# Performance work log

Measured on AMD Instinct MI355X. Metric: run time of the kernel, lower is better.

## Reference

```python
import jax, jax.numpy as jnp
import numpy as np

N, B, T, S, E, R = 4, 8, 512, 512, 1024, 1024


def setup_inputs() -> dict:
    key = jax.random.key(0)
    k1, k2, k3, k4, k5 = jax.random.split(key, 5)
    return {
        "query": jax.random.normal(k1, (1, B, T, E), dtype=jnp.float32),
        "key_value_states": jax.random.normal(k2, (N, B, S, R), dtype=jnp.float32),
        "attention_mask": jax.random.normal(k3, (1, B, T, S), dtype=jnp.float32),
        "Wk": jax.random.normal(k4, (E, R), dtype=jnp.float32) * (1.0 / np.sqrt(R)),
        "bk": jax.random.normal(k5, (E,), dtype=jnp.float32) * 0.01,
    }


def reference(query, key_value_states, attention_mask, Wk, bk):
    # k_proj: [N,B,S,R] @ [R,E] + bias -> [N,B,S,E]
    key = jnp.einsum("nbsr,er->nbse", key_value_states, Wk) + bk
    # QK^T (no scaling), query broadcast over N: [N,B,T,S]
    scores = jnp.einsum("bte,nbse->nbts", query[0], key)
    scores = scores + attention_mask  # mask broadcast over N
    attn = jax.nn.softmax(scores, axis=-1)
    # weights @ raw key_value_states (NOT projected key): [N,B,T,R]
    out = jnp.einsum("nbts,nbsr->nbtr", attn, key_value_states)
    return out
```

## Files before the change

### kernel.cpp

```cpp
#include <hip/hip_runtime.h>

typedef unsigned short u16;
typedef unsigned int u32;
typedef unsigned long long u64;

typedef __bf16 bfrag __attribute__((ext_vector_type(8)));
typedef float f32x4 __attribute__((ext_vector_type(4)));

typedef __attribute__((address_space(1))) char* gas1_p;
typedef __attribute__((address_space(3))) char* las3_p;

#define DI __device__ __forceinline__

DI u16 f2bf(float f) {
  u32 u = __float_as_uint(f);
  u += 0x7FFFu + ((u >> 16) & 1u);
  return (u16)(u >> 16);
}
DI float bf2f(u16 h) { return __uint_as_float(((u32)h) << 16); }

DI void gload16(const void* g, void* l) {
  __builtin_amdgcn_global_load_lds((gas1_p)(u64)g, (las3_p)(u32)(u64)l, 16, 0, 0);
}

__global__ __launch_bounds__(256) void k_split4(const float4* __restrict__ in,
                                                uint2* __restrict__ hi,
                                                uint2* __restrict__ lo) {
  int i = blockIdx.x * 256 + threadIdx.x;
  float4 v = in[i];
  u16 h0 = f2bf(v.x), h1 = f2bf(v.y), h2 = f2bf(v.z), h3 = f2bf(v.w);
  u16 l0 = f2bf(v.x - bf2f(h0)), l1 = f2bf(v.y - bf2f(h1));
  u16 l2 = f2bf(v.z - bf2f(h2)), l3 = f2bf(v.w - bf2f(h3));
  hi[i] = make_uint2((u32)h0 | ((u32)h1 << 16), (u32)h2 | ((u32)h3 << 16));
  lo[i] = make_uint2((u32)l0 | ((u32)l1 << 16), (u32)l2 | ((u32)l3 << 16));
}

template <int WH, int WTH, int WTL>
__global__ __launch_bounds__(256) void k_trsplit64(const float* __restrict__ in,
                                                   u16* __restrict__ hi, u16* __restrict__ lo,
                                                   u16* __restrict__ thi, u16* __restrict__ tlo,
                                                   int rows, int cols) {
  __shared__ float tile[64][65];
  const u64 zoff = (u64)blockIdx.z * (u64)rows * (u64)cols;
  const int r0 = threadIdx.x >> 4;
  const int c4 = (threadIdx.x & 15) << 2;
  const float* src = in + zoff + (u64)(blockIdx.y * 64 + r0) * cols + blockIdx.x * 64 + c4;
#pragma unroll
  for (int p = 0; p < 4; ++p) {
    float4 v = *reinterpret_cast<const float4*>(src + (u64)(p * 16) * cols);
    tile[r0 + p * 16][c4 + 0] = v.x;
    tile[r0 + p * 16][c4 + 1] = v.y;
    tile[r0 + p * 16][c4 + 2] = v.z;
    tile[r0 + p * 16][c4 + 3] = v.w;
  }
  __syncthreads();
  if constexpr (WH) {
    const int rr = threadIdx.x >> 3;
    const int cc = (threadIdx.x & 7) << 3;
#pragma unroll
    for (int p = 0; p < 2; ++p) {
      const int r = rr + p * 32;
      u32 h[4], l[4];
#pragma unroll
      for (int j = 0; j < 4; ++j) {
        float a = tile[r][cc + 2 * j], b = tile[r][cc + 2 * j + 1];
        u16 ha = f2bf(a), hb = f2bf(b);
        h[j] = (u32)ha | ((u32)hb << 16);
        l[j] = (u32)f2bf(a - bf2f(ha)) | ((u32)f2bf(b - bf2f(hb)) << 16);
      }
      const u64 o = zoff + (u64)(blockIdx.y * 64 + r) * cols + blockIdx.x * 64 + cc;
      *reinterpret_cast<uint4*>(hi + o) = make_uint4(h[0], h[1], h[2], h[3]);
      *reinterpret_cast<uint4*>(lo + o) = make_uint4(l[0], l[1], l[2], l[3]);
    }
  }
  if constexpr (WTH) {
#pragma unroll
    for (int p = 0; p < 2; ++p) {
      const int id = threadIdx.x + p * 256;
      const int col = id >> 3;
      const int s8 = (id & 7) << 3;
      u32 h[4], l[4];
#pragma unroll
      for (int j = 0; j < 4; ++j) {
        float a = tile[s8 + 2 * j][col], b = tile[s8 + 2 * j + 1][col];
        u16 ha = f2bf(a), hb = f2bf(b);
        h[j] = (u32)ha | ((u32)hb << 16);
        if constexpr (WTL)
          l[j] = (u32)f2bf(a - bf2f(ha)) | ((u32)f2bf(b - bf2f(hb)) << 16);
      }
      const u64 o = zoff + (u64)(blockIdx.x * 64 + col) * rows + blockIdx.y * 64 + s8;
      *reinterpret_cast<uint4*>(thi + o) = make_uint4(h[0], h[1], h[2], h[3]);
      if constexpr (WTL)
        *reinterpret_cast<uint4*>(tlo + o) = make_uint4(l[0], l[1], l[2], l[3]);
    }
  }
}

template <int X3, int SPLITOUT, int ADDMASK, int XT, int YT>
__global__ __launch_bounds__(256, 2) void k_gemm_bt(
    const u16* __restrict__ Ah, const u16* __restrict__ Al,
    const u16* __restrict__ Bh, const u16* __restrict__ Bl,
    float* __restrict__ Cf, u16* __restrict__ Chi, u16* __restrict__ Clo,
    const float* __restrict__ Mask,
    int K, int N, u64 aStride, int aMask, u64 bStride, u64 cStride) {
  constexpr int OPS = X3 ? 4 : 2;
  __shared__ u16 lds[2][OPS][4096];
  const int tid = threadIdx.x, lane = tid & 63, wid = tid >> 6;

  const int g = (blockIdx.x & 7) * (gridDim.x >> 3) + (blockIdx.x >> 3);
  const int z = g / (XT * YT);
  const int rem = g - z * (XT * YT);
  const int ty = rem / XT, tx = rem - (ty * XT);

  const u64 aOff = (u64)(z & aMask) * aStride;
  const u64 bOff = (u64)z * bStride;
  const u16* gA = Ah + aOff + (u64)ty * 128u * (u32)K;
  const u16* gB = Bh + bOff + (u64)tx * 128u * (u32)K;
  const u16* gAl = nullptr;
  const u16* gBl = nullptr;
  if constexpr (X3) {
    gAl = Al + aOff + (u64)ty * 128u * (u32)K;
    gBl = Bl + bOff + (u64)tx * 128u * (u32)K;
  }
  const int wr = wid >> 1, wc = wid & 1;
  f32x4 acc[4][4];
#pragma unroll
  for (int a = 0; a < 4; ++a)
#pragma unroll
    for (int b = 0; b < 4; ++b) acc[a][b] = (f32x4){0.f, 0.f, 0.f, 0.f};
  const int aFr = (wr * 64 + (lane & 15)) * 32 + (lane >> 4) * 8;
  const int bFr = (wc * 64 + (lane & 15)) * 32 + (lane >> 4) * 8;

  auto STAGE = [&](int buf, int k0) {
#pragma unroll
    for (int call = 0; call < 2; ++call) {
      const int c = call * 256 + tid;
      const u64 gofs = (u64)(c >> 2) * (u32)K + (u32)k0 + (u32)((c & 3) << 3);
      const int lofs = (call * 256 + wid * 64) * 8;
      gload16(gA + gofs, &lds[buf][0][lofs]);
      gload16(gB + gofs, &lds[buf][1][lofs]);
      if constexpr (X3) {
        gload16(gAl + gofs, &lds[buf][2][lofs]);
        gload16(gBl + gofs, &lds[buf][3][lofs]);
      }
    }
  };
  auto COMPUTE = [&](int buf) {
    bfrag ah[4], bh[4], al[4], bl[4];
#pragma unroll
    for (int f = 0; f < 4; ++f) {
      ah[f] = *reinterpret_cast<const bfrag*>(&lds[buf][0][aFr + f * 512]);
      bh[f] = *reinterpret_cast<const bfrag*>(&lds[buf][1][bFr + f * 512]);
      if constexpr (X3) {
        al[f] = *reinterpret_cast<const bfrag*>(&lds[buf][2][aFr + f * 512]);
        bl[f] = *reinterpret_cast<const bfrag*>(&lds[buf][3][bFr + f * 512]);
      }
    }
#pragma unroll
    for (int fm = 0; fm < 4; ++fm)
#pragma unroll
      for (int fn = 0; fn < 4; ++fn) {
        acc[fm][fn] = __builtin_amdgcn_mfma_f32_16x16x32_bf16(ah[fm], bh[fn], acc[fm][fn], 0, 0, 0);
        if constexpr (X3) {
          acc[fm][fn] = __builtin_amdgcn_mfma_f32_16x16x32_bf16(ah[fm], bl[fn], acc[fm][fn], 0, 0, 0);
          acc[fm][fn] = __builtin_amdgcn_mfma_f32_16x16x32_bf16(al[fm], bh[fn], acc[fm][fn], 0, 0, 0);
        }
      }
  };

  STAGE(0, 0);
  __syncthreads();
  int cur = 0;
  for (int k0 = 32; k0 < K; k0 += 32) {
    STAGE(cur ^ 1, k0);
    COMPUTE(cur);
    __syncthreads();
    cur ^= 1;
  }
  COMPUTE(cur);

  const u64 cOff = (u64)z * cStride;
  const u64 mOff = (u64)(z & aMask) * cStride;
  const int rB = ty * 128 + wr * 64 + (lane >> 4) * 4;
  const int cB = tx * 128 + wc * 64 + (lane & 15);
#pragma unroll
  for (int fm = 0; fm < 4; ++fm)
#pragma unroll
    for (int fn = 0; fn < 4; ++fn)
#pragma unroll
      for (int j = 0; j < 4; ++j) {
        const int rr = rB + fm * 16 + j, cc = cB + fn * 16;
        const u64 ci = cOff + (u64)rr * (u32)N + (u32)cc;
        float v = acc[fm][fn][j];
        if constexpr (ADDMASK) v += Mask[mOff + (u64)rr * (u32)N + (u32)cc];
        if constexpr (SPLITOUT) {
          u16 h = f2bf(v);
          Chi[ci] = h;
          Clo[ci] = f2bf(v - bf2f(h));
        } else {
          Cf[ci] = v;
        }
      }
}

__global__ __launch_bounds__(256) void k_softmax(const float* __restrict__ sc,
                                                 u16* __restrict__ attn) {
  const int row = blockIdx.x * 4 + (threadIdx.x >> 6);
  const int lane = threadIdx.x & 63;
  const float* srow = sc + (u64)row * 512 + lane * 8;
  float4 s0 = *reinterpret_cast<const float4*>(srow);
  float4 s1 = *reinterpret_cast<const float4*>(srow + 4);
  float x[8] = {s0.x, s0.y, s0.z, s0.w, s1.x, s1.y, s1.z, s1.w};
  float mx = x[0];
#pragma unroll
  for (int j = 1; j < 8; ++j) mx = fmaxf(mx, x[j]);
#pragma unroll
  for (int off = 32; off > 0; off >>= 1) mx = fmaxf(mx, __shfl_xor(mx, off));
  float sum = 0.f;
#pragma unroll
  for (int j = 0; j < 8; ++j) {
    x[j] = __expf(x[j] - mx);
    sum += x[j];
  }
#pragma unroll
  for (int off = 32; off > 0; off >>= 1) sum += __shfl_xor(sum, off);
  const float inv = 1.f / sum;
  u32 o[4];
#pragma unroll
  for (int j = 0; j < 4; ++j) {
    u16 e0 = f2bf(x[2 * j] * inv), e1 = f2bf(x[2 * j + 1] * inv);
    o[j] = (u32)e0 | ((u32)e1 << 16);
  }
  *reinterpret_cast<uint4*>(attn + (u64)row * 512 + lane * 8) = make_uint4(o[0], o[1], o[2], o[3]);
}

extern "C" void kernel_launch(void* const* d_in, const int* in_sizes, int n_in,
                              void* d_out, int out_size, void* d_ws, size_t ws_size,
                              hipStream_t stream) {
  const float* q = (const float*)d_in[0];
  const float* kvs = (const float*)d_in[1];
  const float* mask = (const float*)d_in[2];
  const float* Wk = (const float*)d_in[3];
  float* out = (float*)d_out;

  char* w = (char*)d_ws;
  u16* q_hi = (u16*)(w + 0);
  u16* q_lo = (u16*)(w + 8388608);
  u16* attn = (u16*)(w + 0);
  u16* wkt_hi = (u16*)(w + 16777216);
  u16* wkt_lo = (u16*)(w + 18874368);
  u16* qp_hi = (u16*)(w + 20971520);
  u16* qp_lo = (u16*)(w + 29360128);
  u16* kv_hi = (u16*)(w + 37748736);
  u16* kv_lo = (u16*)(w + 71303168);
  u16* kvt_hi = (u16*)(w + 104857600);
  float* sc = (float*)(w + 138412032);

  k_split4<<<dim3(4096), dim3(256), 0, stream>>>((const float4*)q, (uint2*)q_hi, (uint2*)q_lo);
  k_trsplit64<0, 1, 1><<<dim3(16, 16, 1), dim3(256), 0, stream>>>(
      Wk, (u16*)nullptr, (u16*)nullptr, wkt_hi, wkt_lo, 1024, 1024);
  k_trsplit64<1, 1, 0><<<dim3(16, 8, 32), dim3(256), 0, stream>>>(
      kvs, kv_hi, kv_lo, kvt_hi, (u16*)nullptr, 512, 1024);
  k_gemm_bt<1, 1, 0, 8, 32><<<dim3(256), dim3(256), 0, stream>>>(
      q_hi, q_lo, wkt_hi, wkt_lo, (float*)nullptr, qp_hi, qp_lo, (const float*)nullptr,
      1024, 1024, (u64)0, 0, (u64)0, (u64)0);
  k_gemm_bt<1, 0, 1, 4, 4><<<dim3(512), dim3(256), 0, stream>>>(
      qp_hi, qp_lo, kv_hi, kv_lo, sc, (u16*)nullptr, (u16*)nullptr, mask,
      1024, 512, (u64)524288, 7, (u64)524288, (u64)262144);
  k_softmax<<<dim3(4096), dim3(256), 0, stream>>>(sc, attn);
  k_gemm_bt<0, 0, 0, 8, 4><<<dim3(1024), dim3(256), 0, stream>>>(
      attn, (u16*)nullptr, kvt_hi, (u16*)nullptr, out, (u16*)nullptr, (u16*)nullptr,
      (const float*)nullptr, 512, 1024, (u64)262144, 31, (u64)524288, (u64)524288);

  (void)in_sizes; (void)n_in; (void)out_size; (void)ws_size;
}
```

Before: 177.0 us.

## Replace GEMM kernel with 8-wave triple-buffered swizzled pipeline

Replaces the 4-wave double-buffered GEMM with a 512-thread kernel that uses three LDS stages, explicit vmcnt waits and raw barriers in place of __syncthreads. It also XOR-swizzles the LDS layout to reduce bank conflicts and raises MFMA issue priority with setprio. Tile shapes change to configurable BM (128 or 256) by 128, so the score and output GEMMs use taller tiles and fewer blocks. The aim is to overlap global loads with MFMA work and cut LDS conflicts. In exchange it uses more LDS and registers, which may lower occupancy, and its correctness rests on the hand-counted vmcnt values.

```diff
diff --git a/kernel.cpp b/kernel.cpp
--- a/kernel.cpp
+++ b/kernel.cpp
@@ -21,6 +21,16 @@
 
 DI void gload16(const void* g, void* l) {
   __builtin_amdgcn_global_load_lds((gas1_p)(u64)g, (las3_p)(u32)(u64)l, 16, 0, 0);
+}
+
+template <int N>
+DI void waitvm() {
+  if constexpr (N >= 12)     asm volatile("s_waitcnt vmcnt(12)" ::: "memory");
+  else if constexpr (N == 8) asm volatile("s_waitcnt vmcnt(8)" ::: "memory");
+  else if constexpr (N == 6) asm volatile("s_waitcnt vmcnt(6)" ::: "memory");
+  else if constexpr (N == 4) asm volatile("s_waitcnt vmcnt(4)" ::: "memory");
+  else if constexpr (N == 3) asm volatile("s_waitcnt vmcnt(3)" ::: "memory");
+  else                       asm volatile("s_waitcnt vmcnt(0)" ::: "memory");
 }
 
 __global__ __launch_bounds__(256) void k_split4(const float4* __restrict__ in,
@@ -96,102 +106,134 @@
   }
 }
 
-template <int X3, int SPLITOUT, int ADDMASK, int XT, int YT>
-__global__ __launch_bounds__(256, 2) void k_gemm_bt(
+template <int X3, int FM, int ADDMASK, int SPLITOUT>
+__global__ __launch_bounds__(512) void k_gemm8(
     const u16* __restrict__ Ah, const u16* __restrict__ Al,
     const u16* __restrict__ Bh, const u16* __restrict__ Bl,
     float* __restrict__ Cf, u16* __restrict__ Chi, u16* __restrict__ Clo,
     const float* __restrict__ Mask,
-    int K, int N, u64 aStride, int aMask, u64 bStride, u64 cStride) {
-  constexpr int OPS = X3 ? 4 : 2;
-  __shared__ u16 lds[2][OPS][4096];
-  const int tid = threadIdx.x, lane = tid & 63, wid = tid >> 6;
+    int K, int N, int mt, int nt,
+    u64 aStride, int aMask, u64 bStride, u64 cStride) {
+  constexpr int BM = FM * 32;
+  constexpr int A_U16 = BM * 32;
+  constexpr int B_U16 = 128 * 32;
+  constexpr int AL0 = A_U16;
+  constexpr int BH0 = A_U16 * (1 + X3);
+  constexpr int BL0 = BH0 + B_U16;
+  constexpr int TILE = (A_U16 + B_U16) * (1 + X3);
+  constexpr int CA = FM / 4;
+  constexpr int L = (CA + 1) * (1 + X3);
+  __shared__ u16 lds[3 * TILE];
+
+  const int tid = threadIdx.x, lane = tid & 63;
+  const int wid = tid >> 6, wr = wid >> 2, wn = wid & 3;
 
   const int g = (blockIdx.x & 7) * (gridDim.x >> 3) + (blockIdx.x >> 3);
-  const int z = g / (XT * YT);
-  const int rem = g - z * (XT * YT);
-  const int ty = rem / XT, tx = rem - (ty * XT);
+  const int z = g / (mt * nt);
+  const int rem = g - z * (mt * nt);
+  const int ty = rem / nt, tx = rem - ty * nt;
 
   const u64 aOff = (u64)(z & aMask) * aStride;
   const u64 bOff = (u64)z * bStride;
-  const u16* gA = Ah + aOff + (u64)ty * 128u * (u32)K;
+  const u16* gA = Ah + aOff + (u64)ty * (u32)BM * (u32)K;
   const u16* gB = Bh + bOff + (u64)tx * 128u * (u32)K;
   const u16* gAl = nullptr;
   const u16* gBl = nullptr;
   if constexpr (X3) {
-    gAl = Al + aOff + (u64)ty * 128u * (u32)K;
+    gAl = Al + aOff + (u64)ty * (u32)BM * (u32)K;
     gBl = Bl + bOff + (u64)tx * 128u * (u32)K;
   }
-  const int wr = wid >> 1, wc = wid & 1;
-  f32x4 acc[4][4];
-#pragma unroll
-  for (int a = 0; a < 4; ++a)
-#pragma unroll
-    for (int b = 0; b < 4; ++b) acc[a][b] = (f32x4){0.f, 0.f, 0.f, 0.f};
-  const int aFr = (wr * 64 + (lane & 15)) * 32 + (lane >> 4) * 8;
-  const int bFr = (wc * 64 + (lane & 15)) * 32 + (lane >> 4) * 8;
-
-  auto STAGE = [&](int buf, int k0) {
-#pragma unroll
-    for (int call = 0; call < 2; ++call) {
-      const int c = call * 256 + tid;
-      const u64 gofs = (u64)(c >> 2) * (u32)K + (u32)k0 + (u32)((c & 3) << 3);
-      const int lofs = (call * 256 + wid * 64) * 8;
-      gload16(gA + gofs, &lds[buf][0][lofs]);
-      gload16(gB + gofs, &lds[buf][1][lofs]);
-      if constexpr (X3) {
-        gload16(gAl + gofs, &lds[buf][2][lofs]);
-        gload16(gBl + gofs, &lds[buf][3][lofs]);
-      }
-    }
+
+  u64 aG[CA];
+  u32 aLo[CA];
+#pragma unroll
+  for (int i = 0; i < CA; ++i) {
+    const int c = i * 512 + tid;
+    const int row = c >> 2, ks = c & 3;
+    aG[i] = (u64)row * (u32)K + (u32)((ks ^ ((row >> 1) & 3)) << 3);
+    aLo[i] = c << 3;
+  }
+  const int rowb = tid >> 2, ksb = tid & 3;
+  const u64 bG = (u64)rowb * (u32)K + (u32)((ksb ^ ((rowb >> 1) & 3)) << 3);
+  const u32 bLo = tid << 3;
+
+  f32x4 acc[FM][2];
+#pragma unroll
+  for (int m = 0; m < FM; ++m)
+#pragma unroll
+    for (int n = 0; n < 2; ++n) acc[m][n] = (f32x4){0.f, 0.f, 0.f, 0.f};
+
+  auto STAGE = [&](int bufU, int k0) {
+#pragma unroll
+    for (int i = 0; i < CA; ++i) {
+      gload16(gA + aG[i] + (u32)k0, &lds[bufU + aLo[i]]);
+      if constexpr (X3) gload16(gAl + aG[i] + (u32)k0, &lds[bufU + AL0 + aLo[i]]);
+    }
+    gload16(gB + bG + (u32)k0, &lds[bufU + BH0 + bLo]);
+    if constexpr (X3) gload16(gBl + bG + (u32)k0, &lds[bufU + BL0 + bLo]);
   };
-  auto COMPUTE = [&](int buf) {
-    bfrag ah[4], bh[4], al[4], bl[4];
-#pragma unroll
-    for (int f = 0; f < 4; ++f) {
-      ah[f] = *reinterpret_cast<const bfrag*>(&lds[buf][0][aFr + f * 512]);
-      bh[f] = *reinterpret_cast<const bfrag*>(&lds[buf][1][bFr + f * 512]);
-      if constexpr (X3) {
-        al[f] = *reinterpret_cast<const bfrag*>(&lds[buf][2][aFr + f * 512]);
-        bl[f] = *reinterpret_cast<const bfrag*>(&lds[buf][3][bFr + f * 512]);
-      }
-    }
-#pragma unroll
-    for (int fm = 0; fm < 4; ++fm)
-#pragma unroll
-      for (int fn = 0; fn < 4; ++fn) {
-        acc[fm][fn] = __builtin_amdgcn_mfma_f32_16x16x32_bf16(ah[fm], bh[fn], acc[fm][fn], 0, 0, 0);
+
+  const int swz = (((lane >> 1) & 3) ^ (lane >> 4)) << 3;
+  auto COMPUTE = [&](int bufU) {
+    bfrag ah[FM], alr[FM], bh[2], blr[2];
+#pragma unroll
+    for (int m = 0; m < FM; ++m) {
+      const int idx = bufU + (wr * (BM / 2) + m * 16 + (lane & 15)) * 32 + swz;
+      ah[m] = *reinterpret_cast<const bfrag*>(&lds[idx]);
+      if constexpr (X3) alr[m] = *reinterpret_cast<const bfrag*>(&lds[idx + AL0]);
+    }
+#pragma unroll
+    for (int n = 0; n < 2; ++n) {
+      const int idx = bufU + BH0 + (wn * 32 + n * 16 + (lane & 15)) * 32 + swz;
+      bh[n] = *reinterpret_cast<const bfrag*>(&lds[idx]);
+      if constexpr (X3) blr[n] = *reinterpret_cast<const bfrag*>(&lds[idx + B_U16]);
+    }
+    __builtin_amdgcn_s_setprio(1);
+#pragma unroll
+    for (int m = 0; m < FM; ++m)
+#pragma unroll
+      for (int n = 0; n < 2; ++n) {
+        acc[m][n] = __builtin_amdgcn_mfma_f32_16x16x32_bf16(ah[m], bh[n], acc[m][n], 0, 0, 0);
         if constexpr (X3) {
-          acc[fm][fn] = __builtin_amdgcn_mfma_f32_16x16x32_bf16(ah[fm], bl[fn], acc[fm][fn], 0, 0, 0);
-          acc[fm][fn] = __builtin_amdgcn_mfma_f32_16x16x32_bf16(al[fm], bh[fn], acc[fm][fn], 0, 0, 0);
+          acc[m][n] = __builtin_amdgcn_mfma_f32_16x16x32_bf16(ah[m], blr[n], acc[m][n], 0, 0, 0);
+          acc[m][n] = __builtin_amdgcn_mfma_f32_16x16x32_bf16(alr[m], bh[n], acc[m][n], 0, 0, 0);
         }
       }
+    __builtin_amdgcn_s_setprio(0);
   };
 
+  const int NT = K >> 5;
   STAGE(0, 0);
-  __syncthreads();
-  int cur = 0;
-  for (int k0 = 32; k0 < K; k0 += 32) {
-    STAGE(cur ^ 1, k0);
-    COMPUTE(cur);
-    __syncthreads();
-    cur ^= 1;
-  }
-  COMPUTE(cur);
+  STAGE(TILE, 32);
+  STAGE(2 * TILE, 64);
+  int buf = 0;
+  for (int t = 0; t < NT; ++t) {
+    const int w = NT - 1 - t;
+    if (w >= 2)      waitvm<2 * L>();
+    else if (w == 1) waitvm<L>();
+    else             waitvm<0>();
+    __builtin_amdgcn_s_barrier();
+    __builtin_amdgcn_sched_barrier(0);
+    COMPUTE(buf * TILE);
+    __builtin_amdgcn_s_barrier();
+    __builtin_amdgcn_sched_barrier(0);
+    if (t + 3 < NT) STAGE(buf * TILE, (t + 3) << 5);
+    buf = (buf == 2) ? 0 : buf + 1;
+  }
 
   const u64 cOff = (u64)z * cStride;
   const u64 mOff = (u64)(z & aMask) * cStride;
-  const int rB = ty * 128 + wr * 64 + (lane >> 4) * 4;
-  const int cB = tx * 128 + wc * 64 + (lane & 15);
-#pragma unroll
-  for (int fm = 0; fm < 4; ++fm)
-#pragma unroll
-    for (int fn = 0; fn < 4; ++fn)
+  const int rB = ty * BM + wr * (BM / 2) + (lane >> 4) * 4;
+  const int cB = tx * 128 + wn * 32 + (lane & 15);
+#pragma unroll
+  for (int m = 0; m < FM; ++m)
+#pragma unroll
+    for (int n = 0; n < 2; ++n)
 #pragma unroll
       for (int j = 0; j < 4; ++j) {
-        const int rr = rB + fm * 16 + j, cc = cB + fn * 16;
+        const int rr = rB + m * 16 + j, cc = cB + n * 16;
         const u64 ci = cOff + (u64)rr * (u32)N + (u32)cc;
-        float v = acc[fm][fn][j];
+        float v = acc[m][n][j];
         if constexpr (ADDMASK) v += Mask[mOff + (u64)rr * (u32)N + (u32)cc];
         if constexpr (SPLITOUT) {
           u16 h = f2bf(v);
@@ -261,16 +303,16 @@
       Wk, (u16*)nullptr, (u16*)nullptr, wkt_hi, wkt_lo, 1024, 1024);
   k_trsplit64<1, 1, 0><<<dim3(16, 8, 32), dim3(256), 0, stream>>>(
       kvs, kv_hi, kv_lo, kvt_hi, (u16*)nullptr, 512, 1024);
-  k_gemm_bt<1, 1, 0, 8, 32><<<dim3(256), dim3(256), 0, stream>>>(
+  k_gemm8<1, 4, 0, 1><<<dim3(256), dim3(512), 0, stream>>>(
       q_hi, q_lo, wkt_hi, wkt_lo, (float*)nullptr, qp_hi, qp_lo, (const float*)nullptr,
-      1024, 1024, (u64)0, 0, (u64)0, (u64)0);
-  k_gemm_bt<1, 0, 1, 4, 4><<<dim3(512), dim3(256), 0, stream>>>(
+      1024, 1024, 32, 8, (u64)0, 0, (u64)0, (u64)0);
+  k_gemm8<1, 8, 1, 0><<<dim3(256), dim3(512), 0, stream>>>(
       qp_hi, qp_lo, kv_hi, kv_lo, sc, (u16*)nullptr, (u16*)nullptr, mask,
-      1024, 512, (u64)524288, 7, (u64)524288, (u64)262144);
+      1024, 512, 2, 4, (u64)524288, 7, (u64)524288, (u64)262144);
   k_softmax<<<dim3(4096), dim3(256), 0, stream>>>(sc, attn);
-  k_gemm_bt<0, 0, 0, 8, 4><<<dim3(1024), dim3(256), 0, stream>>>(
+  k_gemm8<0, 8, 0, 0><<<dim3(512), dim3(512), 0, stream>>>(
       attn, (u16*)nullptr, kvt_hi, (u16*)nullptr, out, (u16*)nullptr, (u16*)nullptr,
-      (const float*)nullptr, 512, 1024, (u64)262144, 31, (u64)524288, (u64)524288);
+      (const float*)nullptr, 512, 1024, 2, 8, (u64)262144, 31, (u64)524288, (u64)524288);
 
   (void)in_sizes; (void)n_in; (void)out_size; (void)ws_size;
 }
```

Result: no change. 176.0 us (-0.5%).
